# Kernel optimization log

Hardware: AMD Instinct MI355X
Metric: run time of the kernel (lower is better)

## Reference

```python
import jax, jax.numpy as jnp
import numpy as np

D_MODEL = 1024
NUM_HEADS = 16
D_HEAD = D_MODEL // NUM_HEADS
BATCH, SEQ, MEM = 2, 1024, 1024
TOT = SEQ + MEM


def setup_inputs() -> dict:
    key = jax.random.key(0)
    ks = jax.random.split(key, 16)
    s = 0.02
    return {
        "x": jax.random.normal(ks[0], (BATCH, SEQ, D_MODEL), jnp.float32),
        "mem": jax.random.normal(ks[1], (BATCH, MEM, D_MODEL), jnp.float32),
        "mask": jnp.zeros((1, 1, SEQ, TOT), jnp.float32),
        "rel_enc": jax.random.normal(ks[2], (TOT, D_MODEL), jnp.float32),
        "Wq": jax.random.normal(ks[3], (D_MODEL, D_MODEL), jnp.float32) * s,
        "bq": jnp.zeros((D_MODEL,), jnp.float32),
        "Wke": jax.random.normal(ks[4], (D_MODEL, D_MODEL), jnp.float32) * s,
        "bke": jnp.zeros((D_MODEL,), jnp.float32),
        "Wkr": jax.random.normal(ks[5], (D_MODEL, D_MODEL), jnp.float32) * s,
        "bkr": jnp.zeros((D_MODEL,), jnp.float32),
        "Wv": jax.random.normal(ks[6], (D_MODEL, D_MODEL), jnp.float32) * s,
        "bv": jnp.zeros((D_MODEL,), jnp.float32),
        "Wo": jax.random.normal(ks[7], (D_MODEL, D_MODEL), jnp.float32) * s,
        "bo": jnp.zeros((D_MODEL,), jnp.float32),
    }


def _split_heads(t, b):
    # (b, s, d_model) -> (b, h, s, d_head)
    return t.reshape(b, -1, NUM_HEADS, D_HEAD).transpose(0, 2, 1, 3)


def _rel_enc_shift(arr):
    # arr: (b, h, l, m) -> Transformer-XL shift trick
    b, h, l, m = arr.shape
    arr = jnp.concatenate([arr, jnp.zeros((b, h, l, 1), arr.dtype)], axis=-1)
    arr = arr.reshape(b, h, l * (m + 1))
    return arr[:, :, l - 1:-1].reshape(b, h, l, m)


def reference(x, mem, mask, rel_enc, Wq, bq, Wke, bke, Wkr, bkr, Wv, bv, Wo, bo):
    b, s, _ = x.shape
    x_tilde = jnp.concatenate([mem, x], axis=1)  # (b, tot, d)
    q = _split_heads(x @ Wq + bq, b)             # (b, h, s, dh)
    k = _split_heads(x_tilde @ Wke + bke, b)     # (b, h, tot, dh)
    v = _split_heads(x_tilde @ Wv + bv, b)       # (b, h, tot, dh)
    A = jnp.einsum("bhsd,bhtd->bhst", q, k)      # content scores
    Q = (rel_enc @ Wkr + bkr).reshape(-1, NUM_HEADS, D_HEAD).transpose(1, 0, 2)  # (h, tot, dh)
    B_hat = jnp.einsum("bhsd,htd->bhst", q, Q)
    B = _rel_enc_shift(B_hat)                    # relative-position scores
    scores = (A + B) / jnp.sqrt(jnp.float32(D_HEAD)) + mask * -1e9
    w = jax.nn.softmax(scores, axis=-1)
    out = jnp.einsum("bhst,bhtd->bhsd", w, v)
    out = out.transpose(0, 2, 1, 3).reshape(b, s, D_MODEL)
    return out @ Wo + bo
```

## Files before the change

### kernel.cpp

```cpp
#include <hip/hip_runtime.h>

typedef unsigned short ushort;
typedef unsigned int uint;
typedef __attribute__((ext_vector_type(8))) short short8;
typedef __attribute__((ext_vector_type(4))) float float4v;

#define D_MODEL 1024
#define NH 16
#define DH 64
#define BATCH 2
#define SEQ 1024
#define MEMLEN 1024
#define TOT 2048

__device__ __forceinline__ float b2f(ushort u) {
  return __uint_as_float(((uint)u) << 16);
}
__device__ __forceinline__ ushort f2b(float f) {
  uint i = __float_as_uint(f);
  uint r = (i + 0x7fffu + ((i >> 16) & 1u)) >> 16;
  return (ushort)r;
}
__device__ __forceinline__ void gld16(const ushort* g, ushort* l) {
  __builtin_amdgcn_global_load_lds(
      (const __attribute__((address_space(1))) void*)g,
      (__attribute__((address_space(3))) void*)l, 16, 0, 0);
}

__global__ __launch_bounds__(256) void concat_cvt_kernel(
    const float* __restrict__ x, const float* __restrict__ mem,
    ushort* __restrict__ xt, ushort* __restrict__ xb) {
  int idx = blockIdx.x * 256 + threadIdx.x;
  int row = idx >> 7;
  int c8 = (idx & 127) << 3;
  int b = row >> 11;
  int i = row & 2047;
  const float* src = (i < MEMLEN) ? &mem[((b << 10) + i) * D_MODEL]
                                  : &x[((b << 10) + (i - MEMLEN)) * D_MODEL];
  float4 f0 = *(const float4*)(&src[c8]);
  float4 f1 = *(const float4*)(&src[c8 + 4]);
  ushort u[8] = {f2b(f0.x), f2b(f0.y), f2b(f0.z), f2b(f0.w),
                 f2b(f1.x), f2b(f1.y), f2b(f1.z), f2b(f1.w)};
  *(uint4*)(&xt[row * D_MODEL + c8]) = *(const uint4*)u;
  if (i >= MEMLEN)
    *(uint4*)(&xb[((b << 10) + (i - MEMLEN)) * D_MODEL + c8]) = *(const uint4*)u;
}

__global__ __launch_bounds__(256) void cvt_kernel(const float* __restrict__ in,
                                                  ushort* __restrict__ out) {
  int idx = blockIdx.x * 256 + threadIdx.x;
  int base = idx << 3;
  float4 f0 = *(const float4*)(&in[base]);
  float4 f1 = *(const float4*)(&in[base + 4]);
  ushort u[8] = {f2b(f0.x), f2b(f0.y), f2b(f0.z), f2b(f0.w),
                 f2b(f1.x), f2b(f1.y), f2b(f1.z), f2b(f1.w)};
  *(uint4*)(&out[base]) = *(const uint4*)u;
}

__global__ __launch_bounds__(256) void maskcvt_kernel(
    const float* __restrict__ in, ushort* __restrict__ out) {
  int idx = blockIdx.x * 256 + threadIdx.x;
  int base = idx << 3;
  float4 f0 = *(const float4*)(&in[base]);
  float4 f1 = *(const float4*)(&in[base + 4]);
  ushort u[8] = {f2b(f0.x * -1e9f), f2b(f0.y * -1e9f), f2b(f0.z * -1e9f),
                 f2b(f0.w * -1e9f), f2b(f1.x * -1e9f), f2b(f1.y * -1e9f),
                 f2b(f1.z * -1e9f), f2b(f1.w * -1e9f)};
  *(uint4*)(&out[base]) = *(const uint4*)u;
}

__global__ __launch_bounds__(256) void transpose_cvt5_kernel(
    const float* __restrict__ W0, const float* __restrict__ W1,
    const float* __restrict__ W2, const float* __restrict__ W3,
    const float* __restrict__ W4, ushort* __restrict__ T0,
    ushort* __restrict__ T1, ushort* __restrict__ T2, ushort* __restrict__ T3,
    ushort* __restrict__ T4) {
  __shared__ ushort tle[32][33];
  const float* W;
  ushort* T;
  switch (blockIdx.z) {
    case 0: W = W0; T = T0; break;
    case 1: W = W1; T = T1; break;
    case 2: W = W2; T = T2; break;
    case 3: W = W3; T = T3; break;
    default: W = W4; T = T4; break;
  }
  const int bx = blockIdx.x * 32, by = blockIdx.y * 32;
  const int tx = threadIdx.x & 31, ty = threadIdx.x >> 5;
#pragma unroll
  for (int j = 0; j < 32; j += 8)
    tle[ty + j][tx] = f2b(W[(by + ty + j) * 1024 + bx + tx]);
  __syncthreads();
#pragma unroll
  for (int j = 0; j < 32; j += 8)
    T[(bx + ty + j) * 1024 + by + tx] = tle[tx][ty + j];
}

__global__ __launch_bounds__(256) void vtrans_kernel(
    const ushort* __restrict__ kv, ushort* __restrict__ vt) {
  __shared__ ushort tle[32][76];
  const int gx = blockIdx.x;
  const int gy = blockIdx.y;
  const int tid = threadIdx.x;
  const int r = tid >> 3, c8 = (tid & 7) * 8;
  *(uint4*)(&tle[r][c8]) =
      *(const uint4*)(&kv[(gx * 32 + r) * 2048 + 1024 + gy * 64 + c8]);
  __syncthreads();
  const int dr = tid >> 2, tc8 = (tid & 3) * 8;
  const int bb = (gx * 32) >> 11, tbase = (gx * 32) & 2047;
  ushort tmp[8];
#pragma unroll
  for (int j = 0; j < 8; ++j) tmp[j] = tle[tc8 + j][dr];
  *(uint4*)(&vt[((bb << 10) + gy * 64 + dr) * 2048 + tbase + tc8]) =
      *(const uint4*)tmp;
}

__global__ __launch_bounds__(256) void gemm_fused_kernel(
    const ushort* __restrict__ xt, const ushort* __restrict__ xbrel,
    const ushort* __restrict__ WkeT, const ushort* __restrict__ WqT,
    const ushort* __restrict__ WkrT, const float* __restrict__ bke,
    const float* __restrict__ bv, const float* __restrict__ bq,
    const float* __restrict__ bkr, ushort* __restrict__ kv,
    ushort* __restrict__ qr) {
  __shared__ ushort As[128 * 32];
  __shared__ ushort Bs[128 * 32];
  const int bid = blockIdx.x;
  const bool seg0 = (bid < 512);
  const ushort* A;
  const ushort* BT;
  ushort* C;
  int ldC, m0, n0;
  if (seg0) {
    m0 = (bid & 31) * 128;
    n0 = (bid >> 5) * 128;
    A = xt;
    BT = WkeT;
    C = kv;
    ldC = 2048;
  } else {
    int g = bid - 512;
    m0 = (g & 31) * 128;
    n0 = (g >> 5) * 128;
    A = xbrel;
    BT = (m0 < 2048) ? WqT : WkrT;
    C = qr;
    ldC = 1024;
  }
  const int tid = threadIdx.x;
  const int w = tid >> 6, lane = tid & 63, m15 = lane & 15, q4 = lane >> 4;
  const int wm = w & 1, wn = w >> 1;
  float4v acc[4][4] = {};
  const int c0 = tid, c1 = tid + 256;
  const int r0 = c0 >> 2, u0 = (c0 & 3) * 8;
  const int r1 = c1 >> 2, u1 = (c1 & 3) * 8;

  for (int kk = 0; kk < 1024; kk += 32) {
    __syncthreads();
    gld16(&A[(m0 + r0) * 1024 + kk + u0], &As[c0 * 8]);
    gld16(&A[(m0 + r1) * 1024 + kk + u1], &As[c1 * 8]);
    gld16(&BT[(n0 + r0) * 1024 + kk + u0], &Bs[c0 * 8]);
    gld16(&BT[(n0 + r1) * 1024 + kk + u1], &Bs[c1 * 8]);
    __syncthreads();
    short8 af[4], bf[4];
#pragma unroll
    for (int i = 0; i < 4; ++i)
      af[i] = *(const short8*)(&As[(wm * 64 + i * 16 + m15) * 32 + q4 * 8]);
#pragma unroll
    for (int j = 0; j < 4; ++j)
      bf[j] = *(const short8*)(&Bs[(wn * 64 + j * 16 + m15) * 32 + q4 * 8]);
#pragma unroll
    for (int i = 0; i < 4; ++i)
#pragma unroll
      for (int j = 0; j < 4; ++j)
        acc[i][j] =
            __builtin_amdgcn_mfma_f32_16x16x32_bf16(af[i], bf[j], acc[i][j], 0, 0, 0);
  }
#pragma unroll
  for (int j = 0; j < 4; ++j) {
    int col = n0 + wn * 64 + j * 16 + m15;
    float bb, sc;
    if (seg0) {
      bb = (col < 1024) ? bke[col] : bv[col - 1024];
      sc = (col < 1024) ? 0.125f : 1.0f;
    } else {
      bb = (m0 < 2048) ? bq[col] : bkr[col];
      sc = (m0 < 2048) ? 1.0f : 0.125f;
    }
#pragma unroll
    for (int i = 0; i < 4; ++i) {
      int rowb = m0 + wm * 64 + i * 16 + q4 * 4;
#pragma unroll
      for (int r = 0; r < 4; ++r)
        C[(rowb + r) * ldC + col] = f2b((acc[i][j][r] + bb) * sc);
    }
  }
}

template <int EPI>
__global__ __launch_bounds__(256) void gemm64_kernel(
    const ushort* __restrict__ A, const ushort* __restrict__ BT,
    const float* __restrict__ bias, void* __restrict__ Cout, int M, int N,
    int K) {
  __shared__ ushort As[64 * 32];
  __shared__ ushort Bs[128 * 32];
  const int m0 = blockIdx.x * 64, n0 = blockIdx.y * 128;
  const int tid = threadIdx.x;
  const int w = tid >> 6, lane = tid & 63, m15 = lane & 15, q4 = lane >> 4;
  float4v acc[4][2] = {};
  const int ra = tid >> 2, ua = (tid & 3) * 8;
  const int c0 = tid, c1 = tid + 256;
  const int rb0 = c0 >> 2, ub0 = (c0 & 3) * 8;
  const int rb1 = c1 >> 2, ub1 = (c1 & 3) * 8;

  for (int kk = 0; kk < K; kk += 32) {
    __syncthreads();
    gld16(&A[(m0 + ra) * K + kk + ua], &As[tid * 8]);
    gld16(&BT[(n0 + rb0) * K + kk + ub0], &Bs[c0 * 8]);
    gld16(&BT[(n0 + rb1) * K + kk + ub1], &Bs[c1 * 8]);
    __syncthreads();
    short8 bf[2];
#pragma unroll
    for (int j = 0; j < 2; ++j)
      bf[j] = *(const short8*)(&Bs[(w * 32 + j * 16 + m15) * 32 + q4 * 8]);
#pragma unroll
    for (int i = 0; i < 4; ++i) {
      short8 af = *(const short8*)(&As[(i * 16 + m15) * 32 + q4 * 8]);
#pragma unroll
      for (int j = 0; j < 2; ++j)
        acc[i][j] =
            __builtin_amdgcn_mfma_f32_16x16x32_bf16(af, bf[j], acc[i][j], 0, 0, 0);
    }
  }
#pragma unroll
  for (int j = 0; j < 2; ++j) {
    int col = n0 + w * 32 + j * 16 + m15;
    float bv = bias[col];
#pragma unroll
    for (int i = 0; i < 4; ++i) {
      int rowb = m0 + i * 16 + q4 * 4;
#pragma unroll
      for (int r = 0; r < 4; ++r) {
        float v = acc[i][j][r] + bv;
        if (EPI == 1)
          ((float*)Cout)[(rowb + r) * N + col] = v;
        else
          ((ushort*)Cout)[(rowb + r) * N + col] = f2b(v);
      }
    }
  }
}

__global__ __launch_bounds__(256) void bhat_kernel(
    const ushort* __restrict__ q, const ushort* __restrict__ Qrb,
    const ushort* __restrict__ maskb, ushort* __restrict__ Bh) {
  __shared__ ushort As[2 * 128 * 32];
  __shared__ ushort Bs[2 * 128 * 32];
  const int bs0 = blockIdx.x * 128, u0 = blockIdx.y * 128, h = blockIdx.z;
  const int tid = threadIdx.x;
  const int w = tid >> 6, lane = tid & 63, m15 = lane & 15, q4 = lane >> 4;
  const int wm = w & 1, wn = w >> 1;

#pragma unroll
  for (int c = 0; c < 4; ++c) {
    int unit = c * 256 + tid;
    int row = (unit >> 2) & 127, kh = unit >> 9, cu = unit & 3;
    gld16(&q[(bs0 + row) * 1024 + (h << 6) + kh * 32 + cu * 8], &As[unit * 8]);
    gld16(&Qrb[(u0 + row) * 1024 + (h << 6) + kh * 32 + cu * 8], &Bs[unit * 8]);
  }
  __syncthreads();

  float4v acc[4][4] = {};
#pragma unroll
  for (int kh = 0; kh < 2; ++kh) {
    short8 af[4], bf[4];
#pragma unroll
    for (int i = 0; i < 4; ++i)
      af[i] = *(const short8*)(&As[kh * 4096 + (wm * 64 + i * 16 + m15) * 32 + q4 * 8]);
#pragma unroll
    for (int j = 0; j < 4; ++j)
      bf[j] = *(const short8*)(&Bs[kh * 4096 + (wn * 64 + j * 16 + m15) * 32 + q4 * 8]);
#pragma unroll
    for (int i = 0; i < 4; ++i)
#pragma unroll
      for (int j = 0; j < 4; ++j)
        acc[i][j] =
            __builtin_amdgcn_mfma_f32_16x16x32_bf16(af[i], bf[j], acc[i][j], 0, 0, 0);
  }
  const int b = bs0 >> 10;
  const int s0loc = bs0 & 1023;
  const int outrow0 = ((b << 4) + h) * 1024 + s0loc;
#pragma unroll
  for (int j = 0; j < 4; ++j) {
    int u = u0 + wn * 64 + j * 16 + m15;
#pragma unroll
    for (int i = 0; i < 4; ++i) {
      int rowb = outrow0 + wm * 64 + i * 16 + q4 * 4;
      int spb = s0loc + wm * 64 + i * 16 + q4 * 4;
#pragma unroll
      for (int r = 0; r < 4; ++r) {
        int sp = spb + r;
        bool selA = (u >= 1023 - sp);
        int mrow = selA ? sp : (sp > 0 ? sp - 1 : 0);
        int mcol = selA ? (u + sp - 1023) : (u + sp + 1025);
        float mval = b2f(maskb[mrow * 2048 + mcol]);
        Bh[(rowb + r) * 2048 + u] = f2b(acc[i][j][r] + mval);
      }
    }
  }
}

__global__ __launch_bounds__(256) void attn_kernel(
    const ushort* __restrict__ qb, const ushort* __restrict__ kv,
    const ushort* __restrict__ vt, const ushort* __restrict__ Bh,
    const ushort* __restrict__ maskb, ushort* __restrict__ attn) {
  __shared__ ushort Pp[4][16 * 36];
  __shared__ float comb[3][16][68];
  __shared__ float csum[3][16];

  const int tid = threadIdx.x;
  const int w = tid >> 6, lane = tid & 63, m15 = lane & 15, q4 = lane >> 4;
  const int th = w;
  const int s0w = blockIdx.x * 16;
  const int h = blockIdx.y, b = blockIdx.z;
  const int s_l = q4 * 4;

  const ushort* qp = &qb[((b << 10) + s0w + m15) * 1024 + (h << 6) + q4 * 8];
  const short8 af0 = *(const short8*)qp;
  const short8 af1 = *(const short8*)(qp + 32);

  const ushort* kvb = &kv[((size_t)(b << 11) * 2048) + (h << 6)];
  const ushort* vtb = &vt[((size_t)((b << 10) + (h << 6))) * 2048];
  const int bhbase = ((b << 4) + h) << 21;
  ushort* pw = &Pp[w][0];

  int offA[4], offB[4], diagT[4];
  float dm[4];
#pragma unroll
  for (int i = 0; i < 4; ++i) {
    int s = s0w + s_l + i;
    offA[i] = bhbase + (s << 11) - s + 1023;
    offB[i] = bhbase + ((s + 1) << 11) - s - 1026;
    diagT[i] = s + 1025;
    dm[i] = (diagT[i] <= 2047) ? b2f(maskb[s * 2048 + diagT[i]]) : 0.f;
  }

  float lsum4[4] = {0.f, 0.f, 0.f, 0.f};
  float4v oacc[4] = {};
  ushort Bb0[8], Bb1[8], Bb2[8], Bb3[8];

  auto pre_bh = [&](int t0, ushort (&B)[8]) {
#pragma unroll
    for (int nt = 0; nt < 2; ++nt)
#pragma unroll
      for (int i = 0; i < 4; ++i) {
        int t = t0 + nt * 16 + m15;
        int off = (t < diagT[i]) ? offA[i] : offB[i];
        B[nt * 4 + i] = Bh[off + t];
      }
  };

  auto phase = [&](int t0, ushort (&Bb)[8], bool pf) {
    short8 Vr[4], Kr[2][2];
#pragma unroll
    for (int nd = 0; nd < 4; ++nd)
      Vr[nd] = *(const short8*)(&vtb[(size_t)(nd * 16 + m15) * 2048 + t0 + q4 * 8]);
#pragma unroll
    for (int nt = 0; nt < 2; ++nt) {
      const ushort* kp = &kvb[(size_t)(t0 + nt * 16 + m15) * 2048 + q4 * 8];
      Kr[nt][0] = *(const short8*)kp;
      Kr[nt][1] = *(const short8*)(kp + 32);
    }
    ushort cur[8];
#pragma unroll
    for (int j = 0; j < 8; ++j) cur[j] = Bb[j];
    if (pf) pre_bh(t0 + 128, Bb);
    float4v a0 = {}, a1 = {};
    a0 = __builtin_amdgcn_mfma_f32_16x16x32_bf16(af0, Kr[0][0], a0, 0, 0, 0);
    a0 = __builtin_amdgcn_mfma_f32_16x16x32_bf16(af1, Kr[0][1], a0, 0, 0, 0);
    a1 = __builtin_amdgcn_mfma_f32_16x16x32_bf16(af0, Kr[1][0], a1, 0, 0, 0);
    a1 = __builtin_amdgcn_mfma_f32_16x16x32_bf16(af1, Kr[1][1], a1, 0, 0, 0);
#pragma unroll
    for (int nt = 0; nt < 2; ++nt)
#pragma unroll
      for (int i = 0; i < 4; ++i) {
        int t = t0 + nt * 16 + m15;
        float bv = (t == diagT[i]) ? dm[i] : b2f(cur[nt * 4 + i]);
        float a = (nt == 0) ? a0[i] : a1[i];
        float p = __expf(a + bv);
        lsum4[i] += p;
        pw[(s_l + i) * 36 + nt * 16 + m15] = f2b(p);
      }
    short8 pfr = *(const short8*)(&pw[m15 * 36 + q4 * 8]);
#pragma unroll
    for (int nd = 0; nd < 4; ++nd)
      oacc[nd] =
          __builtin_amdgcn_mfma_f32_16x16x32_bf16(pfr, Vr[nd], oacc[nd], 0, 0, 0);
  };

  const int tb = th * 512;
  pre_bh(tb, Bb0);
  pre_bh(tb + 32, Bb1);
  pre_bh(tb + 64, Bb2);
  pre_bh(tb + 96, Bb3);
  for (int it = 0; it < 4; ++it) {
    const int t0 = tb + it * 128;
    const bool pf = (it < 3);
    phase(t0, Bb0, pf);
    phase(t0 + 32, Bb1, pf);
    phase(t0 + 64, Bb2, pf);
    phase(t0 + 96, Bb3, pf);
  }

#pragma unroll
  for (int i = 0; i < 4; ++i) {
    float v = lsum4[i];
    v += __shfl_xor(v, 1, 64);
    v += __shfl_xor(v, 2, 64);
    v += __shfl_xor(v, 4, 64);
    v += __shfl_xor(v, 8, 64);
    lsum4[i] = v;
  }
  if (th > 0) {
#pragma unroll
    for (int nd = 0; nd < 4; ++nd)
#pragma unroll
      for (int i = 0; i < 4; ++i)
        comb[th - 1][s_l + i][nd * 16 + m15] = oacc[nd][i];
    if (m15 == 0)
#pragma unroll
      for (int i = 0; i < 4; ++i) csum[th - 1][s_l + i] = lsum4[i];
  }
  __syncthreads();
  if (th == 0) {
#pragma unroll
    for (int i = 0; i < 4; ++i)
      lsum4[i] += csum[0][s_l + i] + csum[1][s_l + i] + csum[2][s_l + i];
#pragma unroll
    for (int nd = 0; nd < 4; ++nd)
#pragma unroll
      for (int i = 0; i < 4; ++i) {
        float v = oacc[nd][i] + comb[0][s_l + i][nd * 16 + m15] +
                  comb[1][s_l + i][nd * 16 + m15] +
                  comb[2][s_l + i][nd * 16 + m15];
        attn[((b << 10) + s0w + s_l + i) * 1024 + (h << 6) + nd * 16 + m15] =
            f2b(v / lsum4[i]);
      }
  }
}

extern "C" void kernel_launch(void* const* d_in, const int* in_sizes, int n_in,
                              void* d_out, int out_size, void* d_ws,
                              size_t ws_size, hipStream_t stream) {
  const float* x = (const float*)d_in[0];
  const float* mem = (const float*)d_in[1];
  const float* mask = (const float*)d_in[2];
  const float* rel = (const float*)d_in[3];
  const float* Wq = (const float*)d_in[4];
  const float* bq = (const float*)d_in[5];
  const float* Wke = (const float*)d_in[6];
  const float* bke = (const float*)d_in[7];
  const float* Wkr = (const float*)d_in[8];
  const float* bkr = (const float*)d_in[9];
  const float* Wv = (const float*)d_in[10];
  const float* bv = (const float*)d_in[11];
  const float* Wo = (const float*)d_in[12];
  const float* bo = (const float*)d_in[13];
  float* out = (float*)d_out;

  ushort* ws = (ushort*)d_ws;
  ushort* xt = ws;
  ushort* xbrel = xt + 4096 * 1024;
  ushort* WqT = xbrel + 4096 * 1024;
  ushort* WkeT = WqT + 1024 * 1024;
  ushort* WvT = WkeT + 1024 * 1024;
  ushort* WkrT = WvT + 1024 * 1024;
  ushort* WoT = WkrT + 1024 * 1024;
  ushort* kv = WoT + 1024 * 1024;
  ushort* qr = kv + 4096 * 2048;
  ushort* attn = qr + 4096 * 1024;
  ushort* maskb = attn + 2048 * 1024;
  ushort* Bh = maskb + 1024 * 2048;
  ushort* relb = xbrel + 2048 * 1024;
  ushort* Qrb = qr + 2048 * 1024;
  ushort* vt = xt;

  concat_cvt_kernel<<<2048, 256, 0, stream>>>(x, mem, xt, xbrel);
  cvt_kernel<<<1024, 256, 0, stream>>>(rel, relb);
  maskcvt_kernel<<<1024, 256, 0, stream>>>(mask, maskb);
  transpose_cvt5_kernel<<<dim3(32, 32, 5), 256, 0, stream>>>(
      Wq, Wke, Wkr, Wv, Wo, WqT, WkeT, WkrT, WvT, WoT);

  gemm_fused_kernel<<<768, 256, 0, stream>>>(xt, xbrel, WkeT, WqT, WkrT, bke,
                                             bv, bq, bkr, kv, qr);
  vtrans_kernel<<<dim3(128, 16), 256, 0, stream>>>(kv, vt);

  bhat_kernel<<<dim3(16, 16, 16), 256, 0, stream>>>(qr, Qrb, maskb, Bh);

  attn_kernel<<<dim3(SEQ / 16, NH, BATCH), 256, 0, stream>>>(
      qr, kv, vt, Bh, maskb, attn);

  gemm64_kernel<1><<<dim3(32, 8), 256, 0, stream>>>(attn, WoT, bo, out, 2048,
                                                    1024, 1024);
}
```

Before: 373.0 us.

## Fuse preprocessing kernels, write V transposed from GEMM epilogue, restructure attention work split

Merges the three conversion kernels into one launch, and drops the separate V transpose kernel by having the projection GEMM epilogue write V directly in a transposed layout inside the kv buffer. The attention kernel now handles two 16-row query tiles per block, each split over two key halves instead of four, which halves the grid and the cross-wave reduction. It also packs the relative-position bias prefetch into uint registers and software-pipelines the K/V loads with sched barriers. The costs are strided 8-byte epilogue stores for V, longer per-wave loops, and fewer blocks in the attention launch.

New measurement: 372.4 us. Within noise of the previous version (-0.2%).

```diff
diff --git a/kernel.cpp b/kernel.cpp
--- a/kernel.cpp
+++ b/kernel.cpp
@@ -27,46 +27,46 @@
       (__attribute__((address_space(3))) void*)l, 16, 0, 0);
 }
 
-__global__ __launch_bounds__(256) void concat_cvt_kernel(
+__global__ __launch_bounds__(256) void preproc_kernel(
     const float* __restrict__ x, const float* __restrict__ mem,
-    ushort* __restrict__ xt, ushort* __restrict__ xb) {
-  int idx = blockIdx.x * 256 + threadIdx.x;
-  int row = idx >> 7;
-  int c8 = (idx & 127) << 3;
-  int b = row >> 11;
-  int i = row & 2047;
-  const float* src = (i < MEMLEN) ? &mem[((b << 10) + i) * D_MODEL]
-                                  : &x[((b << 10) + (i - MEMLEN)) * D_MODEL];
-  float4 f0 = *(const float4*)(&src[c8]);
-  float4 f1 = *(const float4*)(&src[c8 + 4]);
-  ushort u[8] = {f2b(f0.x), f2b(f0.y), f2b(f0.z), f2b(f0.w),
-                 f2b(f1.x), f2b(f1.y), f2b(f1.z), f2b(f1.w)};
-  *(uint4*)(&xt[row * D_MODEL + c8]) = *(const uint4*)u;
-  if (i >= MEMLEN)
-    *(uint4*)(&xb[((b << 10) + (i - MEMLEN)) * D_MODEL + c8]) = *(const uint4*)u;
-}
-
-__global__ __launch_bounds__(256) void cvt_kernel(const float* __restrict__ in,
-                                                  ushort* __restrict__ out) {
-  int idx = blockIdx.x * 256 + threadIdx.x;
-  int base = idx << 3;
-  float4 f0 = *(const float4*)(&in[base]);
-  float4 f1 = *(const float4*)(&in[base + 4]);
-  ushort u[8] = {f2b(f0.x), f2b(f0.y), f2b(f0.z), f2b(f0.w),
-                 f2b(f1.x), f2b(f1.y), f2b(f1.z), f2b(f1.w)};
-  *(uint4*)(&out[base]) = *(const uint4*)u;
-}
-
-__global__ __launch_bounds__(256) void maskcvt_kernel(
-    const float* __restrict__ in, ushort* __restrict__ out) {
-  int idx = blockIdx.x * 256 + threadIdx.x;
-  int base = idx << 3;
-  float4 f0 = *(const float4*)(&in[base]);
-  float4 f1 = *(const float4*)(&in[base + 4]);
-  ushort u[8] = {f2b(f0.x * -1e9f), f2b(f0.y * -1e9f), f2b(f0.z * -1e9f),
-                 f2b(f0.w * -1e9f), f2b(f1.x * -1e9f), f2b(f1.y * -1e9f),
-                 f2b(f1.z * -1e9f), f2b(f1.w * -1e9f)};
-  *(uint4*)(&out[base]) = *(const uint4*)u;
+    const float* __restrict__ rel, const float* __restrict__ mask,
+    ushort* __restrict__ xt, ushort* __restrict__ xb,
+    ushort* __restrict__ relb, ushort* __restrict__ maskb) {
+  const int bid = blockIdx.x;
+  if (bid < 2048) {
+    int idx = bid * 256 + threadIdx.x;
+    int row = idx >> 7;
+    int c8 = (idx & 127) << 3;
+    int b = row >> 11;
+    int i = row & 2047;
+    const float* src = (i < MEMLEN) ? &mem[((b << 10) + i) * D_MODEL]
+                                    : &x[((b << 10) + (i - MEMLEN)) * D_MODEL];
+    float4 f0 = *(const float4*)(&src[c8]);
+    float4 f1 = *(const float4*)(&src[c8 + 4]);
+    ushort u[8] = {f2b(f0.x), f2b(f0.y), f2b(f0.z), f2b(f0.w),
+                   f2b(f1.x), f2b(f1.y), f2b(f1.z), f2b(f1.w)};
+    *(uint4*)(&xt[row * D_MODEL + c8]) = *(const uint4*)u;
+    if (i >= MEMLEN)
+      *(uint4*)(&xb[((b << 10) + (i - MEMLEN)) * D_MODEL + c8]) =
+          *(const uint4*)u;
+  } else if (bid < 3072) {
+    int idx = (bid - 2048) * 256 + threadIdx.x;
+    int base = idx << 3;
+    float4 f0 = *(const float4*)(&rel[base]);
+    float4 f1 = *(const float4*)(&rel[base + 4]);
+    ushort u[8] = {f2b(f0.x), f2b(f0.y), f2b(f0.z), f2b(f0.w),
+                   f2b(f1.x), f2b(f1.y), f2b(f1.z), f2b(f1.w)};
+    *(uint4*)(&relb[base]) = *(const uint4*)u;
+  } else {
+    int idx = (bid - 3072) * 256 + threadIdx.x;
+    int base = idx << 3;
+    float4 f0 = *(const float4*)(&mask[base]);
+    float4 f1 = *(const float4*)(&mask[base + 4]);
+    ushort u[8] = {f2b(f0.x * -1e9f), f2b(f0.y * -1e9f), f2b(f0.z * -1e9f),
+                   f2b(f0.w * -1e9f), f2b(f1.x * -1e9f), f2b(f1.y * -1e9f),
+                   f2b(f1.z * -1e9f), f2b(f1.w * -1e9f)};
+    *(uint4*)(&maskb[base]) = *(const uint4*)u;
+  }
 }
 
 __global__ __launch_bounds__(256) void transpose_cvt5_kernel(
@@ -96,25 +96,6 @@
     T[(bx + ty + j) * 1024 + by + tx] = tle[tx][ty + j];
 }
 
-__global__ __launch_bounds__(256) void vtrans_kernel(
-    const ushort* __restrict__ kv, ushort* __restrict__ vt) {
-  __shared__ ushort tle[32][76];
-  const int gx = blockIdx.x;
-  const int gy = blockIdx.y;
-  const int tid = threadIdx.x;
-  const int r = tid >> 3, c8 = (tid & 7) * 8;
-  *(uint4*)(&tle[r][c8]) =
-      *(const uint4*)(&kv[(gx * 32 + r) * 2048 + 1024 + gy * 64 + c8]);
-  __syncthreads();
-  const int dr = tid >> 2, tc8 = (tid & 3) * 8;
-  const int bb = (gx * 32) >> 11, tbase = (gx * 32) & 2047;
-  ushort tmp[8];
-#pragma unroll
-  for (int j = 0; j < 8; ++j) tmp[j] = tle[tc8 + j][dr];
-  *(uint4*)(&vt[((bb << 10) + gy * 64 + dr) * 2048 + tbase + tc8]) =
-      *(const uint4*)tmp;
-}
-
 __global__ __launch_bounds__(256) void gemm_fused_kernel(
     const ushort* __restrict__ xt, const ushort* __restrict__ xbrel,
     const ushort* __restrict__ WkeT, const ushort* __restrict__ WqT,
@@ -128,23 +109,18 @@
   const bool seg0 = (bid < 512);
   const ushort* A;
   const ushort* BT;
-  ushort* C;
-  int ldC, m0, n0;
+  int m0, n0;
   if (seg0) {
     m0 = (bid & 31) * 128;
     n0 = (bid >> 5) * 128;
     A = xt;
     BT = WkeT;
-    C = kv;
-    ldC = 2048;
   } else {
     int g = bid - 512;
     m0 = (g & 31) * 128;
     n0 = (g >> 5) * 128;
     A = xbrel;
     BT = (m0 < 2048) ? WqT : WkrT;
-    C = qr;
-    ldC = 1024;
   }
   const int tid = threadIdx.x;
   const int w = tid >> 6, lane = tid & 63, m15 = lane & 15, q4 = lane >> 4;
@@ -178,20 +154,41 @@
 #pragma unroll
   for (int j = 0; j < 4; ++j) {
     int col = n0 + wn * 64 + j * 16 + m15;
-    float bb, sc;
     if (seg0) {
-      bb = (col < 1024) ? bke[col] : bv[col - 1024];
-      sc = (col < 1024) ? 0.125f : 1.0f;
+      if (col < 1024) {
+        float bb = bke[col];
+#pragma unroll
+        for (int i = 0; i < 4; ++i) {
+          int rowb = m0 + wm * 64 + i * 16 + q4 * 4;
+#pragma unroll
+          for (int r = 0; r < 4; ++r)
+            kv[(rowb + r) * 2048 + col] = f2b((acc[i][j][r] + bb) * 0.125f);
+        }
+      } else {
+        float bb = bv[col - 1024];
+#pragma unroll
+        for (int i = 0; i < 4; ++i) {
+          int rowb = m0 + wm * 64 + i * 16 + q4 * 4;
+          int dg = ((rowb >> 11) << 10) + (col - 1024);
+          size_t prow = (size_t)(dg * 2 + ((rowb >> 10) & 1)) * 2048 + 1024 +
+                        (rowb & 1023);
+          uint lo = (uint)f2b(acc[i][j][0] + bb) |
+                    ((uint)f2b(acc[i][j][1] + bb) << 16);
+          uint hi = (uint)f2b(acc[i][j][2] + bb) |
+                    ((uint)f2b(acc[i][j][3] + bb) << 16);
+          *(uint2*)(&kv[prow]) = make_uint2(lo, hi);
+        }
+      }
     } else {
-      bb = (m0 < 2048) ? bq[col] : bkr[col];
-      sc = (m0 < 2048) ? 1.0f : 0.125f;
-    }
-#pragma unroll
-    for (int i = 0; i < 4; ++i) {
-      int rowb = m0 + wm * 64 + i * 16 + q4 * 4;
-#pragma unroll
-      for (int r = 0; r < 4; ++r)
-        C[(rowb + r) * ldC + col] = f2b((acc[i][j][r] + bb) * sc);
+      float bb = (m0 < 2048) ? bq[col] : bkr[col];
+      float sc = (m0 < 2048) ? 1.0f : 0.125f;
+#pragma unroll
+      for (int i = 0; i < 4; ++i) {
+        int rowb = m0 + wm * 64 + i * 16 + q4 * 4;
+#pragma unroll
+        for (int r = 0; r < 4; ++r)
+          qr[(rowb + r) * 1024 + col] = f2b((acc[i][j][r] + bb) * sc);
+      }
     }
   }
 }
@@ -311,16 +308,16 @@
 
 __global__ __launch_bounds__(256) void attn_kernel(
     const ushort* __restrict__ qb, const ushort* __restrict__ kv,
-    const ushort* __restrict__ vt, const ushort* __restrict__ Bh,
-    const ushort* __restrict__ maskb, ushort* __restrict__ attn) {
+    const ushort* __restrict__ Bh, const ushort* __restrict__ maskb,
+    ushort* __restrict__ attn) {
   __shared__ ushort Pp[4][16 * 36];
-  __shared__ float comb[3][16][68];
-  __shared__ float csum[3][16];
+  __shared__ float comb[2][16][68];
+  __shared__ float csum[32];
 
   const int tid = threadIdx.x;
   const int w = tid >> 6, lane = tid & 63, m15 = lane & 15, q4 = lane >> 4;
-  const int th = w;
-  const int s0w = blockIdx.x * 16;
+  const int st = w & 1, th = w >> 1;
+  const int s0w = blockIdx.x * 32 + st * 16;
   const int h = blockIdx.y, b = blockIdx.z;
   const int s_l = q4 * 4;
 
@@ -329,7 +326,8 @@
   const short8 af1 = *(const short8*)(qp + 32);
 
   const ushort* kvb = &kv[((size_t)(b << 11) * 2048) + (h << 6)];
-  const ushort* vtb = &vt[((size_t)((b << 10) + (h << 6))) * 2048];
+  const ushort* vrowb =
+      &kv[((size_t)(((b << 10) + (h << 6)) << 1) + th) * 2048 + 1024];
   const int bhbase = ((b << 4) + h) << 21;
   ushort* pw = &Pp[w][0];
 
@@ -346,34 +344,39 @@
 
   float lsum4[4] = {0.f, 0.f, 0.f, 0.f};
   float4v oacc[4] = {};
-  ushort Bb0[8], Bb1[8], Bb2[8], Bb3[8];
-
-  auto pre_bh = [&](int t0, ushort (&B)[8]) {
+
+  auto pre_bh = [&](int t0, uint (&B)[4]) {
 #pragma unroll
     for (int nt = 0; nt < 2; ++nt)
 #pragma unroll
-      for (int i = 0; i < 4; ++i) {
-        int t = t0 + nt * 16 + m15;
-        int off = (t < diagT[i]) ? offA[i] : offB[i];
-        B[nt * 4 + i] = Bh[off + t];
+      for (int ip = 0; ip < 2; ++ip) {
+        uint pk = 0;
+#pragma unroll
+        for (int k = 0; k < 2; ++k) {
+          int i = ip * 2 + k;
+          int t = t0 + nt * 16 + m15;
+          int off = (t < diagT[i]) ? offA[i] : offB[i];
+          ushort v = Bh[off + t];
+          pk |= ((uint)v) << (16 * k);
+        }
+        B[nt * 2 + ip] = pk;
       }
   };
 
-  auto phase = [&](int t0, ushort (&Bb)[8], bool pf) {
-    short8 Vr[4], Kr[2][2];
-#pragma unroll
-    for (int nd = 0; nd < 4; ++nd)
-      Vr[nd] = *(const short8*)(&vtb[(size_t)(nd * 16 + m15) * 2048 + t0 + q4 * 8]);
+  auto loadKV = [&](int t0, short8 (&Kr)[2][2], short8 (&Vr)[4]) {
 #pragma unroll
     for (int nt = 0; nt < 2; ++nt) {
       const ushort* kp = &kvb[(size_t)(t0 + nt * 16 + m15) * 2048 + q4 * 8];
       Kr[nt][0] = *(const short8*)kp;
       Kr[nt][1] = *(const short8*)(kp + 32);
     }
-    ushort cur[8];
-#pragma unroll
-    for (int j = 0; j < 8; ++j) cur[j] = Bb[j];
-    if (pf) pre_bh(t0 + 128, Bb);
+    int tc = (t0 & 1023) + q4 * 8;
+#pragma unroll
+    for (int nd = 0; nd < 4; ++nd)
+      Vr[nd] = *(const short8*)(&vrowb[(size_t)(nd * 16 + m15) * 4096 + tc]);
+  };
+
+  auto work = [&](int t0, short8 (&Kr)[2][2], short8 (&Vr)[4], uint (&B)[4]) {
     float4v a0 = {}, a1 = {};
     a0 = __builtin_amdgcn_mfma_f32_16x16x32_bf16(af0, Kr[0][0], a0, 0, 0, 0);
     a0 = __builtin_amdgcn_mfma_f32_16x16x32_bf16(af1, Kr[0][1], a0, 0, 0, 0);
@@ -384,7 +387,9 @@
 #pragma unroll
       for (int i = 0; i < 4; ++i) {
         int t = t0 + nt * 16 + m15;
-        float bv = (t == diagT[i]) ? dm[i] : b2f(cur[nt * 4 + i]);
+        uint u = B[nt * 2 + (i >> 1)];
+        uint bits = (i & 1) ? (u & 0xffff0000u) : (u << 16);
+        float bv = (t == diagT[i]) ? dm[i] : __uint_as_float(bits);
         float a = (nt == 0) ? a0[i] : a1[i];
         float p = __expf(a + bv);
         lsum4[i] += p;
@@ -397,18 +402,38 @@
           __builtin_amdgcn_mfma_f32_16x16x32_bf16(pfr, Vr[nd], oacc[nd], 0, 0, 0);
   };
 
-  const int tb = th * 512;
+  const int tb = th * 1024;
+  uint Bb0[4], Bb1[4], Bn0[4], Bn1[4];
   pre_bh(tb, Bb0);
   pre_bh(tb + 32, Bb1);
-  pre_bh(tb + 64, Bb2);
-  pre_bh(tb + 96, Bb3);
-  for (int it = 0; it < 4; ++it) {
-    const int t0 = tb + it * 128;
-    const bool pf = (it < 3);
-    phase(t0, Bb0, pf);
-    phase(t0 + 32, Bb1, pf);
-    phase(t0 + 64, Bb2, pf);
-    phase(t0 + 96, Bb3, pf);
+  pre_bh(tb + 64, Bn0);
+  pre_bh(tb + 96, Bn1);
+  for (int p = 0; p < 16; ++p) {
+    const int t0 = tb + p * 64;
+    short8 K0[2][2], V0[4], K1[2][2], V1[4];
+    loadKV(t0, K0, V0);
+    loadKV(t0 + 32, K1, V1);
+    __builtin_amdgcn_sched_barrier(0);
+    uint Bt0[4], Bt1[4];
+    if (p < 14) {
+      pre_bh(t0 + 128, Bt0);
+      pre_bh(t0 + 160, Bt1);
+    }
+    __builtin_amdgcn_sched_barrier(0);
+    work(t0, K0, V0, Bb0);
+    work(t0 + 32, K1, V1, Bb1);
+#pragma unroll
+    for (int j = 0; j < 4; ++j) {
+      Bb0[j] = Bn0[j];
+      Bb1[j] = Bn1[j];
+    }
+    if (p < 14) {
+#pragma unroll
+      for (int j = 0; j < 4; ++j) {
+        Bn0[j] = Bt0[j];
+        Bn1[j] = Bt1[j];
+      }
+    }
   }
 
 #pragma unroll
@@ -420,28 +445,25 @@
     v += __shfl_xor(v, 8, 64);
     lsum4[i] = v;
   }
-  if (th > 0) {
+  if (th == 1) {
 #pragma unroll
     for (int nd = 0; nd < 4; ++nd)
 #pragma unroll
       for (int i = 0; i < 4; ++i)
-        comb[th - 1][s_l + i][nd * 16 + m15] = oacc[nd][i];
+        comb[st][s_l + i][nd * 16 + m15] = oacc[nd][i];
     if (m15 == 0)
 #pragma unroll
-      for (int i = 0; i < 4; ++i) csum[th - 1][s_l + i] = lsum4[i];
+      for (int i = 0; i < 4; ++i) csum[st * 16 + s_l + i] = lsum4[i];
   }
   __syncthreads();
   if (th == 0) {
 #pragma unroll
-    for (int i = 0; i < 4; ++i)
-      lsum4[i] += csum[0][s_l + i] + csum[1][s_l + i] + csum[2][s_l + i];
+    for (int i = 0; i < 4; ++i) lsum4[i] += csum[st * 16 + s_l + i];
 #pragma unroll
     for (int nd = 0; nd < 4; ++nd)
 #pragma unroll
       for (int i = 0; i < 4; ++i) {
-        float v = oacc[nd][i] + comb[0][s_l + i][nd * 16 + m15] +
-                  comb[1][s_l + i][nd * 16 + m15] +
-                  comb[2][s_l + i][nd * 16 + m15];
+        float v = oacc[nd][i] + comb[st][s_l + i][nd * 16 + m15];
         attn[((b << 10) + s0w + s_l + i) * 1024 + (h << 6) + nd * 16 + m15] =
             f2b(v / lsum4[i]);
       }
@@ -482,22 +504,19 @@
   ushort* Bh = maskb + 1024 * 2048;
   ushort* relb = xbrel + 2048 * 1024;
   ushort* Qrb = qr + 2048 * 1024;
-  ushort* vt = xt;
-
-  concat_cvt_kernel<<<2048, 256, 0, stream>>>(x, mem, xt, xbrel);
-  cvt_kernel<<<1024, 256, 0, stream>>>(rel, relb);
-  maskcvt_kernel<<<1024, 256, 0, stream>>>(mask, maskb);
+
+  preproc_kernel<<<4096, 256, 0, stream>>>(x, mem, rel, mask, xt, xbrel, relb,
+                                           maskb);
   transpose_cvt5_kernel<<<dim3(32, 32, 5), 256, 0, stream>>>(
       Wq, Wke, Wkr, Wv, Wo, WqT, WkeT, WkrT, WvT, WoT);
 
   gemm_fused_kernel<<<768, 256, 0, stream>>>(xt, xbrel, WkeT, WqT, WkrT, bke,
                                              bv, bq, bkr, kv, qr);
-  vtrans_kernel<<<dim3(128, 16), 256, 0, stream>>>(kv, vt);
 
   bhat_kernel<<<dim3(16, 16, 16), 256, 0, stream>>>(qr, Qrb, maskb, Bh);
 
-  attn_kernel<<<dim3(SEQ / 16, NH, BATCH), 256, 0, stream>>>(
-      qr, kv, vt, Bh, maskb, attn);
+  attn_kernel<<<dim3(SEQ / 32, NH, BATCH), 256, 0, stream>>>(qr, kv, Bh, maskb,
+                                                             attn);
 
   gemm64_kernel<1><<<dim3(32, 8), 256, 0, stream>>>(attn, WoT, bo, out, 2048,
                                                     1024, 1024);
```
